# Kernel tuning notes

Measured on AMD Instinct MI355X. Metric: run time of the kernel, lower is better.

The kernel has to match this reference:

```python
import jax, jax.numpy as jnp
import numpy as np


def _conv2d(x, w, b, pad):
    out = jax.lax.conv_general_dilated(
        x, w, window_strides=(1, 1), padding=[(pad, pad), (pad, pad)],
        dimension_numbers=("NCHW", "OIHW", "NCHW"))
    return out + b[None, :, None, None]


def _bilinear_sample(x, py, px):
    # x: [B,C,H,W]; py, px: [B,K,H,W] float sample coords -> [B,C,K,H,W]
    B, C, H, W = x.shape
    y0 = jnp.floor(py)
    x0 = jnp.floor(px)
    y1 = y0 + 1.0
    x1 = x0 + 1.0
    wy1 = py - y0
    wy0 = 1.0 - wy1
    wx1 = px - x0
    wx0 = 1.0 - wx1
    xf = x.reshape(B, C, H * W)

    def corner(yc, xc, wgt):
        valid = (yc >= 0) & (yc <= H - 1) & (xc >= 0) & (xc <= W - 1)
        yi = jnp.clip(yc, 0, H - 1).astype(jnp.int32)
        xi = jnp.clip(xc, 0, W - 1).astype(jnp.int32)
        idx = yi * W + xi                      # [B,K,H,W]
        g = jax.vmap(lambda f, i: f[:, i.reshape(-1)])(xf, idx)  # [B,C,K*H*W]
        g = g.reshape(B, C, idx.shape[1], H, W)
        return g * (wgt * valid)[:, None]      # zero weight outside image

    return (corner(y0, x0, wy0 * wx0) + corner(y0, x1, wy0 * wx1)
            + corner(y1, x0, wy1 * wx0) + corner(y1, x1, wy1 * wx1))


def reference(x, c, w_off, b_off, w_dcn, b_dcn):
    # DCNv2Pack forward: conv_offset(c) -> (o1, o2, mask); modulated deform conv on x.
    B, C, H, W = x.shape
    pad, K = 1, 9
    off_out = _conv2d(c, w_off, b_off, pad)            # [B,27,H,W]
    o1, o2, m = jnp.split(off_out, 3, axis=1)
    offset = jnp.concatenate([o1, o2], axis=1)         # [B,18,H,W]
    mask = jax.nn.sigmoid(m)                           # [B,9,H,W]
    # offset channel layout: [dy_0, dx_0, dy_1, dx_1, ...] per kernel tap
    off = offset.reshape(B, K, 2, H, W)
    ky, kx = jnp.meshgrid(jnp.arange(3), jnp.arange(3), indexing="ij")
    ky = (ky.reshape(K) - pad).astype(x.dtype)
    kx = (kx.reshape(K) - pad).astype(x.dtype)
    base_y = jnp.arange(H, dtype=x.dtype).reshape(1, 1, H, 1)
    base_x = jnp.arange(W, dtype=x.dtype).reshape(1, 1, 1, W)
    py = base_y + ky.reshape(1, K, 1, 1) + off[:, :, 0]  # [B,K,H,W]
    px = base_x + kx.reshape(1, K, 1, 1) + off[:, :, 1]
    samp = _bilinear_sample(x, py, px)                 # [B,C,K,H,W]
    samp = samp * mask[:, None]                        # modulation
    C_out = w_dcn.shape[0]
    out = jnp.einsum("bckhw,ock->bohw", samp, w_dcn.reshape(C_out, C, K))
    return out + b_dcn[None, :, None, None]


def setup_inputs():
    key = jax.random.key(0)
    ks = jax.random.split(key, 4)
    B, C, H, W = 4, 64, 128, 128
    x = jax.random.normal(ks[0], (B, C, H, W), jnp.float32)
    c = jax.random.normal(ks[1], (B, C, H, W), jnp.float32)
    # conv_offset is zero-init in DCNv2Pack; use small random weights so
    # offsets are non-trivial but bounded (realistic trained regime).
    w_off = jax.random.normal(ks[2], (27, C, 3, 3), jnp.float32) * 0.01
    b_off = jnp.zeros((27,), jnp.float32)
    w_dcn = jax.random.normal(ks[3], (C, C, 3, 3), jnp.float32) * (1.0 / np.sqrt(C * 9))
    b_dcn = jnp.zeros((C,), jnp.float32)
    return {"x": x, "c": c, "w_off": w_off, "b_off": b_off,
            "w_dcn": w_dcn, "b_dcn": b_dcn}
```

## Files before the change

kernel.cpp:

```cpp
#include <hip/hip_runtime.h>
#include <math.h>

#define BB 4
#define C 64
#define H 128
#define W 128
#define HW (H*W)
#define KC 576
#define XR 6
#define XC 38
#define CR 4
#define CCW 34
#define OFFS 28

typedef __attribute__((ext_vector_type(4))) float f32x4;
typedef __attribute__((ext_vector_type(4))) _Float16 f16x4;
typedef __attribute__((ext_vector_type(8))) _Float16 f16x8;

static __device__ __forceinline__ f16x8 splat8(float f) {
  _Float16 h = (_Float16)f;
  f16x8 v = {h, h, h, h, h, h, h, h};
  return v;
}

__global__ __launch_bounds__(256) void xpose_prep_kernel(
    const float* __restrict__ x, const float* __restrict__ cin,
    const float* __restrict__ wd, const float* __restrict__ woff,
    _Float16* __restrict__ xt, _Float16* __restrict__ ct,
    _Float16* __restrict__ wtbf, _Float16* __restrict__ wotf) {
  __shared__ _Float16 lds16[32 * 72];
  int t = threadIdx.x;

  if (blockIdx.y == 1 && blockIdx.x < 144) {
    int i = blockIdx.x * 256 + t;
    {
      int j = i & 7, ln = (i >> 3) & 63, fi = i >> 9;
      int ot = fi & 3, kb = fi >> 2;
      int o = ot * 16 + (ln & 15);
      int kcol = kb * 32 + (ln >> 4) * 8 + j;
      int k = kcol >> 6, cc = kcol & 63;
      wtbf[i] = (_Float16)wd[(o * C + cc) * 9 + k];
    }
    if (i < 32 * KC) {
      int j = i & 7, ln = (i >> 3) & 63, fi = i >> 9;
      int ot2 = fi & 1, kb = fi >> 1;
      int o = ot2 * 16 + (ln & 15);
      int kcol = kb * 32 + (ln >> 4) * 8 + j;
      int k = kcol >> 6, cc = kcol & 63;
      wotf[i] = (o < 27) ? (_Float16)woff[(o * C + cc) * 9 + k] : (_Float16)0.f;
    }
  }

  const float* src = blockIdx.y ? cin : x;
  _Float16* dst = blockIdx.y ? ct : xt;

  int P0 = blockIdx.x * 32;
  int b = P0 >> 14;
  int pp0 = P0 & (HW - 1);

  int p = t & 31;
  int cg = t >> 5;
  const float* xb = src + (size_t)b * C * HW + pp0 + p;
  f16x8 u;
#pragma unroll
  for (int j = 0; j < 8; ++j)
    u[j] = (_Float16)xb[(cg * 8 + j) * HW];
  *(f16x8*)(lds16 + p * 72 + ((cg ^ (p & 7)) << 3)) = u;

  __syncthreads();

  int q = t >> 3;
  int s = t & 7;
  f16x8 v = *(const f16x8*)(lds16 + q * 72 + ((s ^ (q & 7)) << 3));
  *(f16x8*)(dst + (size_t)(P0 + q) * 64 + s * 8) = v;
}

__global__ __launch_bounds__(256) void dcn_fused_kernel(
    const _Float16* __restrict__ xt, const _Float16* __restrict__ ct,
    const _Float16* __restrict__ wtbf, const _Float16* __restrict__ wotf,
    const float* __restrict__ boff, const float* __restrict__ bd,
    float* __restrict__ out) {
  __shared__ __align__(16) unsigned char smem[32768];
  _Float16* win  = (_Float16*)smem;
  _Float16* offT = (_Float16*)(smem + 29184);

  int tid = threadIdx.x;
  int bid = blockIdx.x;
  int w0 = (bid & 3) * 32;
  int h0 = ((bid >> 2) & 63) * 2;
  int b  = bid >> 8;

  int lane = tid & 63;
  int wv = tid >> 6;
  int lr = lane & 15, lh = lane >> 4;
  int h   = h0 + (wv >> 1);
  int wpx = w0 + (wv & 1) * 16 + lr;

  const _Float16* xtb = xt + (size_t)b * HW * 64;
  const _Float16* ctb = ct + (size_t)b * HW * 64;

  int crlo = min(max(h0 - 1, 0), H - CR);
  int cclo = min(max(w0 - 1, 0), W - CCW);
  int rlo  = min(max(h0 - 2, 0), H - XR);
  int clo  = min(max(w0 - 3, 0), W - XC);

#pragma unroll
  for (int sweep = 0; sweep < 5; ++sweep) {
    int cch = sweep * 256 + tid;
    if (cch < CR * CCW * 8) {
      int pixw = cch >> 3, part = cch & 7;
      int row = pixw / CCW, col = pixw - row * CCW;
      *(f16x8*)(win + (size_t)pixw * 64 + ((part ^ (pixw & 7)) << 3)) =
        *(const f16x8*)(ctb + ((size_t)(crlo + row) * W + cclo + col) * 64 + part * 8);
    }
  }
  __syncthreads();

  f32x4 acc1a = {0.f, 0.f, 0.f, 0.f};
  f32x4 acc1b = {0.f, 0.f, 0.f, 0.f};
#pragma unroll 2
  for (int kb = 0; kb < 18; ++kb) {
    int t9 = kb >> 1;
    int cg = (kb & 1) * 4 + lh;
    int ty = h + t9 / 3 - 1;
    int tx = wpx + t9 % 3 - 1;
    bool okv = (ty >= 0) && (ty < H) && (tx >= 0) && (tx < W);
    int pixw = (min(max(ty, 0), H - 1) - crlo) * CCW
             + (min(max(tx, 0), W - 1) - cclo);
    f16x8 bf = *(const f16x8*)(win + (size_t)pixw * 64 + ((cg ^ (pixw & 7)) << 3));
    if (!okv) bf = splat8(0.f);
    f16x8 a0 = *(const f16x8*)(wotf + ((size_t)(kb * 2 + 0) * 64 + lane) * 8);
    f16x8 a1 = *(const f16x8*)(wotf + ((size_t)(kb * 2 + 1) * 64 + lane) * 8);
    acc1a = __builtin_amdgcn_mfma_f32_16x16x32_f16(a0, bf, acc1a, 0, 0, 0);
    acc1b = __builtin_amdgcn_mfma_f32_16x16x32_f16(a1, bf, acc1b, 0, 0, 0);
  }

  {
    f16x4 v0, v1;
#pragma unroll
    for (int r = 0; r < 4; ++r) {
      int o0 = lh * 4 + r;
      int o1 = 16 + lh * 4 + r;
      v0[r] = (_Float16)(acc1a[r] + boff[o0]);
      v1[r] = (_Float16)(acc1b[r] + ((o1 < 27) ? boff[o1] : 0.f));
    }
    _Float16* base = offT + ((size_t)wv * 16 + lr) * OFFS;
    *(f16x4*)(base + lh * 4) = v0;
    if (lh < 3) *(f16x4*)(base + 16 + lh * 4) = v1;
  }
  __syncthreads();

#pragma unroll
  for (int sweep = 0; sweep < 8; ++sweep) {
    int cch = sweep * 256 + tid;
    if (cch < XR * XC * 8) {
      int pixw = cch >> 3, part = cch & 7;
      int row = pixw / XC, col = pixw - row * XC;
      *(f16x8*)(win + (size_t)pixw * 64 + ((part ^ (pixw & 7)) << 3)) =
        *(const f16x8*)(xtb + ((size_t)(rlo + row) * W + clo + col) * 64 + part * 8);
    }
  }
  f16x4 rvh[7];
#pragma unroll
  for (int j = 0; j < 7; ++j)
    rvh[j] = *(const f16x4*)(offT + ((size_t)wv * 16 + lr) * OFFS + 4 * j);
  __syncthreads();

#define OFFV(i) ((float)rvh[(i) >> 2][(i) & 3])

  f32x4 acc[4];
#pragma unroll
  for (int i = 0; i < 4; ++i) acc[i] = (f32x4){0.f, 0.f, 0.f, 0.f};

#pragma unroll
  for (int k = 0; k < 9; ++k) {
    float dy = OFFV(2 * k);
    float dx = OFFV(2 * k + 1);
    float mv = OFFV(18 + k);
    float m = 1.0f / (1.0f + __expf(-mv));

    float py = (float)(h + k / 3 - 1) + dy;
    float px = (float)(wpx + k % 3 - 1) + dx;
    float y0f = floorf(py), x0f = floorf(px);
    int y0 = (int)y0f, x0 = (int)x0f;
    float wy1 = py - y0f, wx1 = px - x0f;
    float wy0 = 1.0f - wy1, wx0 = 1.0f - wx1;

    bool y0v = (y0 >= 0) && (y0 < H);
    bool y1v = (y0 + 1 >= 0) && (y0 + 1 < H);
    bool x0v = (x0 >= 0) && (x0 < W);
    bool x1v = (x0 + 1 >= 0) && (x0 + 1 < W);
    int y0c = min(max(y0, 0), H - 1), y1c = min(max(y0 + 1, 0), H - 1);
    int x0c = min(max(x0, 0), W - 1), x1c = min(max(x0 + 1, 0), W - 1);

    float w00 = wy0 * wx0 * (float)(y0v && x0v) * m;
    float w01 = wy0 * wx1 * (float)(y0v && x1v) * m;
    float w10 = wy1 * wx0 * (float)(y1v && x0v) * m;
    float w11 = wy1 * wx1 * (float)(y1v && x1v) * m;

    int iy0 = y0c - rlo, iy1 = y1c - rlo;
    int ix0 = x0c - clo, ix1 = x1c - clo;
    bool inY0 = (unsigned)iy0 < XR, inY1 = (unsigned)iy1 < XR;
    bool inX0 = (unsigned)ix0 < XC, inX1 = (unsigned)ix1 < XC;
    bool in00 = inY0 && inX0, in01 = inY0 && inX1;
    bool in10 = inY1 && inX0, in11 = inY1 && inX1;
    int p00 = min(max(iy0, 0), XR - 1) * XC + min(max(ix0, 0), XC - 1);
    int p01 = min(max(iy0, 0), XR - 1) * XC + min(max(ix1, 0), XC - 1);
    int p10 = min(max(iy1, 0), XR - 1) * XC + min(max(ix0, 0), XC - 1);
    int p11 = min(max(iy1, 0), XR - 1) * XC + min(max(ix1, 0), XC - 1);

#pragma unroll
    for (int half = 0; half < 2; ++half) {
      int cg = half * 4 + lh;
      f16x8 c00 = *(const f16x8*)(win + (size_t)p00 * 64 + ((cg ^ (p00 & 7)) << 3));
      f16x8 c01 = *(const f16x8*)(win + (size_t)p01 * 64 + ((cg ^ (p01 & 7)) << 3));
      f16x8 c10 = *(const f16x8*)(win + (size_t)p10 * 64 + ((cg ^ (p10 & 7)) << 3));
      f16x8 c11 = *(const f16x8*)(win + (size_t)p11 * 64 + ((cg ^ (p11 & 7)) << 3));
      if (!in00) c00 = *(const f16x8*)(xtb + ((size_t)y0c * W + x0c) * 64 + cg * 8);
      if (!in01) c01 = *(const f16x8*)(xtb + ((size_t)y0c * W + x1c) * 64 + cg * 8);
      if (!in10) c10 = *(const f16x8*)(xtb + ((size_t)y1c * W + x0c) * 64 + cg * 8);
      if (!in11) c11 = *(const f16x8*)(xtb + ((size_t)y1c * W + x1c) * 64 + cg * 8);

      f16x8 s = c00 * splat8(w00);
      s += c01 * splat8(w01);
      s += c10 * splat8(w10);
      s += c11 * splat8(w11);

      int kb = 2 * k + half;
#pragma unroll
      for (int ot = 0; ot < 4; ++ot) {
        f16x8 a = *(const f16x8*)(wtbf + ((size_t)(kb * 4 + ot) * 64 + lane) * 8);
        acc[ot] = __builtin_amdgcn_mfma_f32_16x16x32_f16(a, s, acc[ot], 0, 0, 0);
      }
    }
  }

#pragma unroll
  for (int ot = 0; ot < 4; ++ot) {
#pragma unroll
    for (int r = 0; r < 4; ++r) {
      int o = ot * 16 + lh * 4 + r;
      size_t base = ((size_t)(b * C + o)) * HW + (size_t)h * W + w0 + (wv & 1) * 16 + lr;
      out[base] = acc[ot][r] + bd[o];
    }
  }
}

extern "C" void kernel_launch(void* const* d_in, const int* in_sizes, int n_in,
                              void* d_out, int out_size, void* d_ws, size_t ws_size,
                              hipStream_t stream) {
  const float* x    = (const float*)d_in[0];
  const float* c    = (const float*)d_in[1];
  const float* woff = (const float*)d_in[2];
  const float* boff = (const float*)d_in[3];
  const float* wdcn = (const float*)d_in[4];
  const float* bdcn = (const float*)d_in[5];
  float* out = (float*)d_out;

  _Float16* xt   = (_Float16*)d_ws;
  _Float16* ct   = xt + 4194304;
  _Float16* wtbf = ct + 4194304;
  _Float16* wotf = wtbf + 36864;

  int npix = BB * H * W;
  dim3 gx(npix / 32, 2);
  xpose_prep_kernel<<<gx, 256, 0, stream>>>(x, c, wdcn, woff, xt, ct, wtbf, wotf);
  dcn_fused_kernel<<<npix / 64, 256, 0, stream>>>(xt, ct, wtbf, wotf, boff, bdcn, out);
}
```

Measured before the change: 39.95 us.

## Drop NHWC fp16 transpose pass; load NCHW fp32 tiles directly into LDS

Removes the separate kernel that converted x and c to channel-last fp16 in workspace. The fused kernel now reads NCHW fp32 tiles straight from global memory, converts them to fp16 and writes the swizzled LDS window. Weight reordering moves to a small prep kernel. This saves one full read-write pass over both inputs. In exchange, halo tiles are re-read in fp32 with strided per-channel loads, and out-of-window corner gathers now need eight scattered loads instead of one vector load.

```diff
diff --git a/kernel.cpp b/kernel.cpp
--- a/kernel.cpp
+++ b/kernel.cpp
@@ -23,60 +23,30 @@
   return v;
 }
 
-__global__ __launch_bounds__(256) void xpose_prep_kernel(
+__global__ __launch_bounds__(256) void prep_kernel(
+    const float* __restrict__ wd, const float* __restrict__ woff,
+    _Float16* __restrict__ wtbf, _Float16* __restrict__ wotf) {
+  int i = blockIdx.x * 256 + threadIdx.x;
+  {
+    int j = i & 7, ln = (i >> 3) & 63, fi = i >> 9;
+    int ot = fi & 3, kb = fi >> 2;
+    int o = ot * 16 + (ln & 15);
+    int kcol = kb * 32 + (ln >> 4) * 8 + j;
+    int k = kcol >> 6, cc = kcol & 63;
+    wtbf[i] = (_Float16)wd[(o * C + cc) * 9 + k];
+  }
+  if (i < 32 * KC) {
+    int j = i & 7, ln = (i >> 3) & 63, fi = i >> 9;
+    int ot2 = fi & 1, kb = fi >> 1;
+    int o = ot2 * 16 + (ln & 15);
+    int kcol = kb * 32 + (ln >> 4) * 8 + j;
+    int k = kcol >> 6, cc = kcol & 63;
+    wotf[i] = (o < 27) ? (_Float16)woff[(o * C + cc) * 9 + k] : (_Float16)0.f;
+  }
+}
+
+__global__ __launch_bounds__(256) void dcn_fused_kernel(
     const float* __restrict__ x, const float* __restrict__ cin,
-    const float* __restrict__ wd, const float* __restrict__ woff,
-    _Float16* __restrict__ xt, _Float16* __restrict__ ct,
-    _Float16* __restrict__ wtbf, _Float16* __restrict__ wotf) {
-  __shared__ _Float16 lds16[32 * 72];
-  int t = threadIdx.x;
-
-  if (blockIdx.y == 1 && blockIdx.x < 144) {
-    int i = blockIdx.x * 256 + t;
-    {
-      int j = i & 7, ln = (i >> 3) & 63, fi = i >> 9;
-      int ot = fi & 3, kb = fi >> 2;
-      int o = ot * 16 + (ln & 15);
-      int kcol = kb * 32 + (ln >> 4) * 8 + j;
-      int k = kcol >> 6, cc = kcol & 63;
-      wtbf[i] = (_Float16)wd[(o * C + cc) * 9 + k];
-    }
-    if (i < 32 * KC) {
-      int j = i & 7, ln = (i >> 3) & 63, fi = i >> 9;
-      int ot2 = fi & 1, kb = fi >> 1;
-      int o = ot2 * 16 + (ln & 15);
-      int kcol = kb * 32 + (ln >> 4) * 8 + j;
-      int k = kcol >> 6, cc = kcol & 63;
-      wotf[i] = (o < 27) ? (_Float16)woff[(o * C + cc) * 9 + k] : (_Float16)0.f;
-    }
-  }
-
-  const float* src = blockIdx.y ? cin : x;
-  _Float16* dst = blockIdx.y ? ct : xt;
-
-  int P0 = blockIdx.x * 32;
-  int b = P0 >> 14;
-  int pp0 = P0 & (HW - 1);
-
-  int p = t & 31;
-  int cg = t >> 5;
-  const float* xb = src + (size_t)b * C * HW + pp0 + p;
-  f16x8 u;
-#pragma unroll
-  for (int j = 0; j < 8; ++j)
-    u[j] = (_Float16)xb[(cg * 8 + j) * HW];
-  *(f16x8*)(lds16 + p * 72 + ((cg ^ (p & 7)) << 3)) = u;
-
-  __syncthreads();
-
-  int q = t >> 3;
-  int s = t & 7;
-  f16x8 v = *(const f16x8*)(lds16 + q * 72 + ((s ^ (q & 7)) << 3));
-  *(f16x8*)(dst + (size_t)(P0 + q) * 64 + s * 8) = v;
-}
-
-__global__ __launch_bounds__(256) void dcn_fused_kernel(
-    const _Float16* __restrict__ xt, const _Float16* __restrict__ ct,
     const _Float16* __restrict__ wtbf, const _Float16* __restrict__ wotf,
     const float* __restrict__ boff, const float* __restrict__ bd,
     float* __restrict__ out) {
@@ -96,22 +66,30 @@
   int h   = h0 + (wv >> 1);
   int wpx = w0 + (wv & 1) * 16 + lr;
 
-  const _Float16* xtb = xt + (size_t)b * HW * 64;
-  const _Float16* ctb = ct + (size_t)b * HW * 64;
+  const float* xb = x   + (size_t)b * C * HW;
+  const float* cb = cin + (size_t)b * C * HW;
 
   int crlo = min(max(h0 - 1, 0), H - CR);
   int cclo = min(max(w0 - 1, 0), W - CCW);
   int rlo  = min(max(h0 - 2, 0), H - XR);
   int clo  = min(max(w0 - 3, 0), W - XC);
 
-#pragma unroll
-  for (int sweep = 0; sweep < 5; ++sweep) {
-    int cch = sweep * 256 + tid;
-    if (cch < CR * CCW * 8) {
-      int pixw = cch >> 3, part = cch & 7;
-      int row = pixw / CCW, col = pixw - row * CCW;
-      *(f16x8*)(win + (size_t)pixw * 64 + ((part ^ (pixw & 7)) << 3)) =
-        *(const f16x8*)(ctb + ((size_t)(crlo + row) * W + cclo + col) * 64 + part * 8);
+  int pg = tid & 31;
+  int cg8 = tid >> 5;
+
+  {
+    const float* src0 = cb + (size_t)(cg8 * 8) * HW;
+#pragma unroll
+    for (int g = 0; g < 5; ++g) {
+      int p = g * 32 + pg;
+      if (p < CR * CCW) {
+        int row = p / CCW, col = p - row * CCW;
+        const float* s = src0 + (size_t)(crlo + row) * W + (cclo + col);
+        f16x8 u;
+#pragma unroll
+        for (int j = 0; j < 8; ++j) u[j] = (_Float16)s[(size_t)j * HW];
+        *(f16x8*)(win + (size_t)p * 64 + ((cg8 ^ (p & 7)) << 3)) = u;
+      }
     }
   }
   __syncthreads();
@@ -150,14 +128,19 @@
   }
   __syncthreads();
 
-#pragma unroll
-  for (int sweep = 0; sweep < 8; ++sweep) {
-    int cch = sweep * 256 + tid;
-    if (cch < XR * XC * 8) {
-      int pixw = cch >> 3, part = cch & 7;
-      int row = pixw / XC, col = pixw - row * XC;
-      *(f16x8*)(win + (size_t)pixw * 64 + ((part ^ (pixw & 7)) << 3)) =
-        *(const f16x8*)(xtb + ((size_t)(rlo + row) * W + clo + col) * 64 + part * 8);
+  {
+    const float* src0 = xb + (size_t)(cg8 * 8) * HW;
+#pragma unroll
+    for (int g = 0; g < 8; ++g) {
+      int p = g * 32 + pg;
+      if (p < XR * XC) {
+        int row = p / XC, col = p - row * XC;
+        const float* s = src0 + (size_t)(rlo + row) * W + (clo + col);
+        f16x8 u;
+#pragma unroll
+        for (int j = 0; j < 8; ++j) u[j] = (_Float16)s[(size_t)j * HW];
+        *(f16x8*)(win + (size_t)p * 64 + ((cg8 ^ (p & 7)) << 3)) = u;
+      }
     }
   }
   f16x4 rvh[7];
@@ -216,10 +199,18 @@
       f16x8 c01 = *(const f16x8*)(win + (size_t)p01 * 64 + ((cg ^ (p01 & 7)) << 3));
       f16x8 c10 = *(const f16x8*)(win + (size_t)p10 * 64 + ((cg ^ (p10 & 7)) << 3));
       f16x8 c11 = *(const f16x8*)(win + (size_t)p11 * 64 + ((cg ^ (p11 & 7)) << 3));
-      if (!in00) c00 = *(const f16x8*)(xtb + ((size_t)y0c * W + x0c) * 64 + cg * 8);
-      if (!in01) c01 = *(const f16x8*)(xtb + ((size_t)y0c * W + x1c) * 64 + cg * 8);
-      if (!in10) c10 = *(const f16x8*)(xtb + ((size_t)y1c * W + x0c) * 64 + cg * 8);
-      if (!in11) c11 = *(const f16x8*)(xtb + ((size_t)y1c * W + x1c) * 64 + cg * 8);
+      if (!in00) { const float* s = xb + (size_t)(cg * 8) * HW + y0c * W + x0c;
+#pragma unroll
+        for (int j = 0; j < 8; ++j) c00[j] = (_Float16)s[(size_t)j * HW]; }
+      if (!in01) { const float* s = xb + (size_t)(cg * 8) * HW + y0c * W + x1c;
+#pragma unroll
+        for (int j = 0; j < 8; ++j) c01[j] = (_Float16)s[(size_t)j * HW]; }
+      if (!in10) { const float* s = xb + (size_t)(cg * 8) * HW + y1c * W + x0c;
+#pragma unroll
+        for (int j = 0; j < 8; ++j) c10[j] = (_Float16)s[(size_t)j * HW]; }
+      if (!in11) { const float* s = xb + (size_t)(cg * 8) * HW + y1c * W + x1c;
+#pragma unroll
+        for (int j = 0; j < 8; ++j) c11[j] = (_Float16)s[(size_t)j * HW]; }
 
       f16x8 s = c00 * splat8(w00);
       s += c01 * splat8(w01);
@@ -257,13 +248,9 @@
   const float* bdcn = (const float*)d_in[5];
   float* out = (float*)d_out;
 
-  _Float16* xt   = (_Float16*)d_ws;
-  _Float16* ct   = xt + 4194304;
-  _Float16* wtbf = ct + 4194304;
+  _Float16* wtbf = (_Float16*)d_ws;
   _Float16* wotf = wtbf + 36864;
 
-  int npix = BB * H * W;
-  dim3 gx(npix / 32, 2);
-  xpose_prep_kernel<<<gx, 256, 0, stream>>>(x, c, wdcn, woff, xt, ct, wtbf, wotf);
-  dcn_fused_kernel<<<npix / 64, 256, 0, stream>>>(xt, ct, wtbf, wotf, boff, bdcn, out);
-}
+  prep_kernel<<<144, 256, 0, stream>>>(wdcn, woff, wtbf, wotf);
+  dcn_fused_kernel<<<(BB * HW) / 64, 256, 0, stream>>>(x, c, wtbf, wotf, boff, bdcn, out);
+}
```

Measured after the change: 48.31 us. +20.9%, slower.

## Shrink fused DCN block to one row with channel-halved LDS windows

Applied to the files above, without the earlier changes.

Each block now covers one output row of 32 pixels instead of two rows. Waves are split across pixel halves and output-channel halves, so each wave holds two accumulators rather than four. The c and x windows are staged into LDS in two 32-channel halves, which halves the shared memory to 16KB, and launch bounds request 6 blocks per CU to raise occupancy. In exchange there are twice as many blocks, more barriers, and more redundant halo loading per output pixel.

```diff
diff --git a/kernel.cpp b/kernel.cpp
--- a/kernel.cpp
+++ b/kernel.cpp
@@ -9,7 +9,7 @@
 #define KC 576
 #define XR 6
 #define XC 38
-#define CR 4
+#define CR 3
 #define CCW 34
 #define OFFS 28
 
@@ -75,151 +75,153 @@
   *(f16x8*)(dst + (size_t)(P0 + q) * 64 + s * 8) = v;
 }
 
-__global__ __launch_bounds__(256) void dcn_fused_kernel(
+__global__ __launch_bounds__(256, 6) void dcn_fused_kernel(
     const _Float16* __restrict__ xt, const _Float16* __restrict__ ct,
     const _Float16* __restrict__ wtbf, const _Float16* __restrict__ wotf,
     const float* __restrict__ boff, const float* __restrict__ bd,
     float* __restrict__ out) {
-  __shared__ __align__(16) unsigned char smem[32768];
+  __shared__ __align__(16) unsigned char smem[16384];
   _Float16* win  = (_Float16*)smem;
-  _Float16* offT = (_Float16*)(smem + 29184);
+  _Float16* offT = (_Float16*)(smem + 14592);
 
   int tid = threadIdx.x;
   int bid = blockIdx.x;
   int w0 = (bid & 3) * 32;
-  int h0 = ((bid >> 2) & 63) * 2;
-  int b  = bid >> 8;
+  int h  = (bid >> 2) & 127;
+  int b  = bid >> 9;
 
   int lane = tid & 63;
   int wv = tid >> 6;
+  int oh = wv & 1;
+  int ph = wv >> 1;
   int lr = lane & 15, lh = lane >> 4;
-  int h   = h0 + (wv >> 1);
-  int wpx = w0 + (wv & 1) * 16 + lr;
+  int wpx = w0 + ph * 16 + lr;
 
   const _Float16* xtb = xt + (size_t)b * HW * 64;
   const _Float16* ctb = ct + (size_t)b * HW * 64;
 
-  int crlo = min(max(h0 - 1, 0), H - CR);
+  int crlo = min(max(h - 1, 0), H - CR);
   int cclo = min(max(w0 - 1, 0), W - CCW);
-  int rlo  = min(max(h0 - 2, 0), H - XR);
+  int rlo  = min(max(h - 2, 0), H - XR);
   int clo  = min(max(w0 - 3, 0), W - XC);
 
-#pragma unroll
-  for (int sweep = 0; sweep < 5; ++sweep) {
-    int cch = sweep * 256 + tid;
-    if (cch < CR * CCW * 8) {
-      int pixw = cch >> 3, part = cch & 7;
-      int row = pixw / CCW, col = pixw - row * CCW;
-      *(f16x8*)(win + (size_t)pixw * 64 + ((part ^ (pixw & 7)) << 3)) =
-        *(const f16x8*)(ctb + ((size_t)(crlo + row) * W + cclo + col) * 64 + part * 8);
-    }
+  f32x4 acc1 = {0.f, 0.f, 0.f, 0.f};
+
+#pragma unroll
+  for (int half = 0; half < 2; ++half) {
+#pragma unroll
+    for (int g = 0; g < 2; ++g) {
+      int cch = g * 256 + tid;
+      if (cch < CR * CCW * 4) {
+        int pixw = cch >> 2, part = cch & 3;
+        int row = pixw / CCW, col = pixw - row * CCW;
+        *(f16x8*)(win + (size_t)pixw * 32 + ((part ^ (pixw & 3)) << 3)) =
+          *(const f16x8*)(ctb + ((size_t)(crlo + row) * W + cclo + col) * 64
+                          + half * 32 + part * 8);
+      }
+    }
+    __syncthreads();
+
+#pragma unroll
+    for (int t9 = 0; t9 < 9; ++t9) {
+      int kb = 2 * t9 + half;
+      int ty = h + t9 / 3 - 1;
+      int tx = wpx + t9 % 3 - 1;
+      bool okv = (ty >= 0) && (ty < H) && (tx >= 0) && (tx < W);
+      int pixw = (min(max(ty, 0), H - 1) - crlo) * CCW
+               + (min(max(tx, 0), W - 1) - cclo);
+      f16x8 bf = *(const f16x8*)(win + (size_t)pixw * 32 + ((lh ^ (pixw & 3)) << 3));
+      if (!okv) bf = splat8(0.f);
+      f16x8 a = *(const f16x8*)(wotf + ((size_t)(kb * 2 + oh) * 64 + lane) * 8);
+      acc1 = __builtin_amdgcn_mfma_f32_16x16x32_f16(a, bf, acc1, 0, 0, 0);
+    }
+    __syncthreads();
+  }
+
+  if (oh == 0 || lh < 3) {
+    f16x4 v;
+#pragma unroll
+    for (int r = 0; r < 4; ++r) {
+      int o = oh * 16 + lh * 4 + r;
+      v[r] = (_Float16)(acc1[r] + ((o < 27) ? boff[o] : 0.f));
+    }
+    *(f16x4*)(offT + ((size_t)ph * 16 + lr) * OFFS + oh * 16 + lh * 4) = v;
   }
   __syncthreads();
 
-  f32x4 acc1a = {0.f, 0.f, 0.f, 0.f};
-  f32x4 acc1b = {0.f, 0.f, 0.f, 0.f};
-#pragma unroll 2
-  for (int kb = 0; kb < 18; ++kb) {
-    int t9 = kb >> 1;
-    int cg = (kb & 1) * 4 + lh;
-    int ty = h + t9 / 3 - 1;
-    int tx = wpx + t9 % 3 - 1;
-    bool okv = (ty >= 0) && (ty < H) && (tx >= 0) && (tx < W);
-    int pixw = (min(max(ty, 0), H - 1) - crlo) * CCW
-             + (min(max(tx, 0), W - 1) - cclo);
-    f16x8 bf = *(const f16x8*)(win + (size_t)pixw * 64 + ((cg ^ (pixw & 7)) << 3));
-    if (!okv) bf = splat8(0.f);
-    f16x8 a0 = *(const f16x8*)(wotf + ((size_t)(kb * 2 + 0) * 64 + lane) * 8);
-    f16x8 a1 = *(const f16x8*)(wotf + ((size_t)(kb * 2 + 1) * 64 + lane) * 8);
-    acc1a = __builtin_amdgcn_mfma_f32_16x16x32_f16(a0, bf, acc1a, 0, 0, 0);
-    acc1b = __builtin_amdgcn_mfma_f32_16x16x32_f16(a1, bf, acc1b, 0, 0, 0);
-  }
-
-  {
-    f16x4 v0, v1;
-#pragma unroll
-    for (int r = 0; r < 4; ++r) {
-      int o0 = lh * 4 + r;
-      int o1 = 16 + lh * 4 + r;
-      v0[r] = (_Float16)(acc1a[r] + boff[o0]);
-      v1[r] = (_Float16)(acc1b[r] + ((o1 < 27) ? boff[o1] : 0.f));
-    }
-    _Float16* base = offT + ((size_t)wv * 16 + lr) * OFFS;
-    *(f16x4*)(base + lh * 4) = v0;
-    if (lh < 3) *(f16x4*)(base + 16 + lh * 4) = v1;
-  }
-  __syncthreads();
-
-#pragma unroll
-  for (int sweep = 0; sweep < 8; ++sweep) {
-    int cch = sweep * 256 + tid;
-    if (cch < XR * XC * 8) {
-      int pixw = cch >> 3, part = cch & 7;
-      int row = pixw / XC, col = pixw - row * XC;
-      *(f16x8*)(win + (size_t)pixw * 64 + ((part ^ (pixw & 7)) << 3)) =
-        *(const f16x8*)(xtb + ((size_t)(rlo + row) * W + clo + col) * 64 + part * 8);
-    }
-  }
-  f16x4 rvh[7];
+  f16x4 rv[7];
 #pragma unroll
   for (int j = 0; j < 7; ++j)
-    rvh[j] = *(const f16x4*)(offT + ((size_t)wv * 16 + lr) * OFFS + 4 * j);
-  __syncthreads();
-
-#define OFFV(i) ((float)rvh[(i) >> 2][(i) & 3])
-
-  f32x4 acc[4];
-#pragma unroll
-  for (int i = 0; i < 4; ++i) acc[i] = (f32x4){0.f, 0.f, 0.f, 0.f};
-
-#pragma unroll
-  for (int k = 0; k < 9; ++k) {
-    float dy = OFFV(2 * k);
-    float dx = OFFV(2 * k + 1);
-    float mv = OFFV(18 + k);
-    float m = 1.0f / (1.0f + __expf(-mv));
-
-    float py = (float)(h + k / 3 - 1) + dy;
-    float px = (float)(wpx + k % 3 - 1) + dx;
-    float y0f = floorf(py), x0f = floorf(px);
-    int y0 = (int)y0f, x0 = (int)x0f;
-    float wy1 = py - y0f, wx1 = px - x0f;
-    float wy0 = 1.0f - wy1, wx0 = 1.0f - wx1;
-
-    bool y0v = (y0 >= 0) && (y0 < H);
-    bool y1v = (y0 + 1 >= 0) && (y0 + 1 < H);
-    bool x0v = (x0 >= 0) && (x0 < W);
-    bool x1v = (x0 + 1 >= 0) && (x0 + 1 < W);
-    int y0c = min(max(y0, 0), H - 1), y1c = min(max(y0 + 1, 0), H - 1);
-    int x0c = min(max(x0, 0), W - 1), x1c = min(max(x0 + 1, 0), W - 1);
-
-    float w00 = wy0 * wx0 * (float)(y0v && x0v) * m;
-    float w01 = wy0 * wx1 * (float)(y0v && x1v) * m;
-    float w10 = wy1 * wx0 * (float)(y1v && x0v) * m;
-    float w11 = wy1 * wx1 * (float)(y1v && x1v) * m;
-
-    int iy0 = y0c - rlo, iy1 = y1c - rlo;
-    int ix0 = x0c - clo, ix1 = x1c - clo;
-    bool inY0 = (unsigned)iy0 < XR, inY1 = (unsigned)iy1 < XR;
-    bool inX0 = (unsigned)ix0 < XC, inX1 = (unsigned)ix1 < XC;
-    bool in00 = inY0 && inX0, in01 = inY0 && inX1;
-    bool in10 = inY1 && inX0, in11 = inY1 && inX1;
-    int p00 = min(max(iy0, 0), XR - 1) * XC + min(max(ix0, 0), XC - 1);
-    int p01 = min(max(iy0, 0), XR - 1) * XC + min(max(ix1, 0), XC - 1);
-    int p10 = min(max(iy1, 0), XR - 1) * XC + min(max(ix0, 0), XC - 1);
-    int p11 = min(max(iy1, 0), XR - 1) * XC + min(max(ix1, 0), XC - 1);
-
-#pragma unroll
-    for (int half = 0; half < 2; ++half) {
-      int cg = half * 4 + lh;
-      f16x8 c00 = *(const f16x8*)(win + (size_t)p00 * 64 + ((cg ^ (p00 & 7)) << 3));
-      f16x8 c01 = *(const f16x8*)(win + (size_t)p01 * 64 + ((cg ^ (p01 & 7)) << 3));
-      f16x8 c10 = *(const f16x8*)(win + (size_t)p10 * 64 + ((cg ^ (p10 & 7)) << 3));
-      f16x8 c11 = *(const f16x8*)(win + (size_t)p11 * 64 + ((cg ^ (p11 & 7)) << 3));
-      if (!in00) c00 = *(const f16x8*)(xtb + ((size_t)y0c * W + x0c) * 64 + cg * 8);
-      if (!in01) c01 = *(const f16x8*)(xtb + ((size_t)y0c * W + x1c) * 64 + cg * 8);
-      if (!in10) c10 = *(const f16x8*)(xtb + ((size_t)y1c * W + x0c) * 64 + cg * 8);
-      if (!in11) c11 = *(const f16x8*)(xtb + ((size_t)y1c * W + x1c) * 64 + cg * 8);
+    rv[j] = *(const f16x4*)(offT + ((size_t)ph * 16 + lr) * OFFS + 4 * j);
+
+#define OFFV(i) ((float)rv[(i) >> 2][(i) & 3])
+
+  f32x4 acc[2];
+  acc[0] = (f32x4){0.f, 0.f, 0.f, 0.f};
+  acc[1] = (f32x4){0.f, 0.f, 0.f, 0.f};
+
+#pragma unroll
+  for (int half = 0; half < 2; ++half) {
+#pragma unroll
+    for (int g = 0; g < 4; ++g) {
+      int cch = g * 256 + tid;
+      if (cch < XR * XC * 4) {
+        int pixw = cch >> 2, part = cch & 3;
+        int row = pixw / XC, col = pixw - row * XC;
+        *(f16x8*)(win + (size_t)pixw * 32 + ((part ^ (pixw & 3)) << 3)) =
+          *(const f16x8*)(xtb + ((size_t)(rlo + row) * W + clo + col) * 64
+                          + half * 32 + part * 8);
+      }
+    }
+    __syncthreads();
+
+    int cgg = half * 4 + lh;
+
+#pragma unroll
+    for (int k = 0; k < 9; ++k) {
+      float dy = OFFV(2 * k);
+      float dx = OFFV(2 * k + 1);
+      float mv = OFFV(18 + k);
+      float m = 1.0f / (1.0f + __expf(-mv));
+
+      float py = (float)(h + k / 3 - 1) + dy;
+      float px = (float)(wpx + k % 3 - 1) + dx;
+      float y0f = floorf(py), x0f = floorf(px);
+      int y0 = (int)y0f, x0 = (int)x0f;
+      float wy1 = py - y0f, wx1 = px - x0f;
+      float wy0 = 1.0f - wy1, wx0 = 1.0f - wx1;
+
+      bool y0v = (y0 >= 0) && (y0 < H);
+      bool y1v = (y0 + 1 >= 0) && (y0 + 1 < H);
+      bool x0v = (x0 >= 0) && (x0 < W);
+      bool x1v = (x0 + 1 >= 0) && (x0 + 1 < W);
+      int y0c = min(max(y0, 0), H - 1), y1c = min(max(y0 + 1, 0), H - 1);
+      int x0c = min(max(x0, 0), W - 1), x1c = min(max(x0 + 1, 0), W - 1);
+
+      float w00 = wy0 * wx0 * (float)(y0v && x0v) * m;
+      float w01 = wy0 * wx1 * (float)(y0v && x1v) * m;
+      float w10 = wy1 * wx0 * (float)(y1v && x0v) * m;
+      float w11 = wy1 * wx1 * (float)(y1v && x1v) * m;
+
+      int iy0 = y0c - rlo, iy1 = y1c - rlo;
+      int ix0 = x0c - clo, ix1 = x1c - clo;
+      bool inY0 = (unsigned)iy0 < XR, inY1 = (unsigned)iy1 < XR;
+      bool inX0 = (unsigned)ix0 < XC, inX1 = (unsigned)ix1 < XC;
+      bool in00 = inY0 && inX0, in01 = inY0 && inX1;
+      bool in10 = inY1 && inX0, in11 = inY1 && inX1;
+      int p00 = min(max(iy0, 0), XR - 1) * XC + min(max(ix0, 0), XC - 1);
+      int p01 = min(max(iy0, 0), XR - 1) * XC + min(max(ix1, 0), XC - 1);
+      int p10 = min(max(iy1, 0), XR - 1) * XC + min(max(ix0, 0), XC - 1);
+      int p11 = min(max(iy1, 0), XR - 1) * XC + min(max(ix1, 0), XC - 1);
+
+      f16x8 c00 = *(const f16x8*)(win + (size_t)p00 * 32 + ((lh ^ (p00 & 3)) << 3));
+      f16x8 c01 = *(const f16x8*)(win + (size_t)p01 * 32 + ((lh ^ (p01 & 3)) << 3));
+      f16x8 c10 = *(const f16x8*)(win + (size_t)p10 * 32 + ((lh ^ (p10 & 3)) << 3));
+      f16x8 c11 = *(const f16x8*)(win + (size_t)p11 * 32 + ((lh ^ (p11 & 3)) << 3));
+      if (!in00) c00 = *(const f16x8*)(xtb + ((size_t)y0c * W + x0c) * 64 + cgg * 8);
+      if (!in01) c01 = *(const f16x8*)(xtb + ((size_t)y0c * W + x1c) * 64 + cgg * 8);
+      if (!in10) c10 = *(const f16x8*)(xtb + ((size_t)y1c * W + x0c) * 64 + cgg * 8);
+      if (!in11) c11 = *(const f16x8*)(xtb + ((size_t)y1c * W + x1c) * 64 + cgg * 8);
 
       f16x8 s = c00 * splat8(w00);
       s += c01 * splat8(w01);
@@ -228,20 +230,21 @@
 
       int kb = 2 * k + half;
 #pragma unroll
-      for (int ot = 0; ot < 4; ++ot) {
-        f16x8 a = *(const f16x8*)(wtbf + ((size_t)(kb * 4 + ot) * 64 + lane) * 8);
-        acc[ot] = __builtin_amdgcn_mfma_f32_16x16x32_f16(a, s, acc[ot], 0, 0, 0);
+      for (int i = 0; i < 2; ++i) {
+        f16x8 a = *(const f16x8*)(wtbf + ((size_t)(kb * 4 + oh * 2 + i) * 64 + lane) * 8);
+        acc[i] = __builtin_amdgcn_mfma_f32_16x16x32_f16(a, s, acc[i], 0, 0, 0);
       }
     }
-  }
-
-#pragma unroll
-  for (int ot = 0; ot < 4; ++ot) {
+    __syncthreads();
+  }
+
+#pragma unroll
+  for (int i = 0; i < 2; ++i) {
 #pragma unroll
     for (int r = 0; r < 4; ++r) {
-      int o = ot * 16 + lh * 4 + r;
-      size_t base = ((size_t)(b * C + o)) * HW + (size_t)h * W + w0 + (wv & 1) * 16 + lr;
-      out[base] = acc[ot][r] + bd[o];
+      int o = (oh * 2 + i) * 16 + lh * 4 + r;
+      size_t base = ((size_t)(b * C + o)) * HW + (size_t)h * W + wpx;
+      out[base] = acc[i][r] + bd[o];
     }
   }
 }
@@ -265,5 +268,5 @@
   int npix = BB * H * W;
   dim3 gx(npix / 32, 2);
   xpose_prep_kernel<<<gx, 256, 0, stream>>>(x, c, wdcn, woff, xt, ct, wtbf, wotf);
-  dcn_fused_kernel<<<npix / 64, 256, 0, stream>>>(xt, ct, wtbf, wotf, boff, bdcn, out);
-}
+  dcn_fused_kernel<<<npix / 32, 256, 0, stream>>>(xt, ct, wtbf, wotf, boff, bdcn, out);
+}
```

After: 141.9 us. 3.55x slower.
